# Kernel tuning notes

Measured on AMD Instinct MI355X. Metric: run time of the kernel, lower is better.

The kernel has to match this reference:

```python
import jax, jax.numpy as jnp
import numpy as np

GRID_SIZE = 5
SPLINE_ORDER = 3
NUM_COEFF = GRID_SIZE + SPLINE_ORDER  # 8
L = 3
B, I, H = 4096, 256, 512
EPS = 1e-5


def make_grid(in_features):
    # efficient-kan default grid over [-1, 1] extended by spline_order knots each side
    h = 2.0 / GRID_SIZE
    g = jnp.arange(-SPLINE_ORDER, GRID_SIZE + SPLINE_ORDER + 1, dtype=jnp.float32) * h - 1.0
    return jnp.broadcast_to(g, (in_features, g.shape[0]))  # (in, G+2k+1)


def b_splines(x, grid):
    # x: (B, in), grid: (in, G+2k+1) -> (B, in, G+k) via Cox-de-Boor recursion
    xg = x[..., None]
    bases = ((xg >= grid[:, :-1]) & (xg < grid[:, 1:])).astype(x.dtype)
    for j in range(1, SPLINE_ORDER + 1):
        left = (xg - grid[:, :-(j + 1)]) / (grid[:, j:-1] - grid[:, :-(j + 1)])
        right = (grid[:, j + 1:] - xg) / (grid[:, j + 1:] - grid[:, 1:-j])
        bases = left * bases[..., :-1] + right * bases[..., 1:]
    return bases


def kan_linear(x, base_w, spline_w, grid):
    # base path: SiLU(x) @ W_base^T ; spline path: sum over (in, coeff)
    base = jax.nn.silu(x) @ base_w.T
    spl = jnp.einsum('bik,oik->bo', b_splines(x, grid), spline_w)
    return base + spl


def layer_norm(x, g, b):
    mu = jnp.mean(x, axis=-1, keepdims=True)
    var = jnp.var(x, axis=-1, keepdims=True)
    return (x - mu) / jnp.sqrt(var + EPS) * g + b


def _sublayer(z_prev, wx_b, wx_s, wh_b, wh_s, hz_b, hz_s, phi_b, phi_s,
              hh_w, hh_b, ln_g, ln_b, x_t, grid_in, grid_h):
    s_t = kan_linear(x_t, wx_b, wx_s, grid_in) + kan_linear(z_prev, wh_b, wh_s, grid_h)
    o_t = kan_linear(s_t, phi_b, phi_s, grid_h)
    z_t = layer_norm(z_prev @ hh_w.T + hh_b + kan_linear(o_t, hz_b, hz_s, grid_h), ln_g, ln_b)
    return o_t, z_t


def setup_inputs() -> dict:
    key = jax.random.key(0)
    ks = jax.random.split(key, 24)
    s = 0.05  # small init to keep gates/splines in sane range
    inp = {
        'x_t': jax.random.normal(ks[0], (B, I), jnp.float32),
        'h_prev': jax.random.normal(ks[1], (B, H), jnp.float32),
        'c_prev': jax.random.normal(ks[2], (B, H), jnp.float32),
        'z_prev': jax.random.normal(ks[3], (L, B, H), jnp.float32),
        'wx_base': jax.random.normal(ks[4], (L, H, I), jnp.float32) * s,
        'wx_spline': jax.random.normal(ks[5], (L, H, I, NUM_COEFF), jnp.float32) * s,
        'wh_base': jax.random.normal(ks[6], (L, H, H), jnp.float32) * s,
        'wh_spline': jax.random.normal(ks[7], (L, H, H, NUM_COEFF), jnp.float32) * s,
        'hz_base': jax.random.normal(ks[8], (L, H, H), jnp.float32) * s,
        'hz_spline': jax.random.normal(ks[9], (L, H, H, NUM_COEFF), jnp.float32) * s,
        'phi_base': jax.random.normal(ks[10], (L, H, H), jnp.float32) * s,
        'phi_spline': jax.random.normal(ks[11], (L, H, H, NUM_COEFF), jnp.float32) * s,
        'hh_w': jax.random.normal(ks[12], (L, H, H), jnp.float32) * s,
        'hh_b': jax.random.normal(ks[13], (L, H), jnp.float32) * s,
        'ln_g': jnp.ones((L, H), jnp.float32),
        'ln_b': jnp.zeros((L, H), jnp.float32),
        'f_w': jax.random.normal(ks[14], (H, I + H), jnp.float32) * s,
        'f_b': jax.random.normal(ks[15], (H,), jnp.float32) * s,
        'i_w': jax.random.normal(ks[16], (H, I + H), jnp.float32) * s,
        'i_b': jax.random.normal(ks[17], (H,), jnp.float32) * s,
        'g_w': jax.random.normal(ks[18], (H, I + H), jnp.float32) * s,
        'g_b': jax.random.normal(ks[19], (H,), jnp.float32) * s,
        'o_w': jax.random.normal(ks[20], (H, L * H), jnp.float32) * s,
        'o_b': jax.random.normal(ks[21], (H,), jnp.float32) * s,
    }
    return inp


def reference(x_t, h_prev, c_prev, z_prev, wx_base, wx_spline, wh_base, wh_spline,
              hz_base, hz_spline, phi_base, phi_spline, hh_w, hh_b, ln_g, ln_b,
              f_w, f_b, i_w, i_b, g_w, g_b, o_w, o_b):
    grid_in = make_grid(I)
    grid_h = make_grid(H)
    cat = jnp.concatenate([x_t, h_prev], axis=-1)  # (B, I+H)
    f_t = jax.nn.sigmoid(cat @ f_w.T + f_b)
    i_t = jax.nn.sigmoid(cat @ i_w.T + i_b)
    g_t = jnp.tanh(cat @ g_w.T + g_b)
    # vmap the RKAN sublayer over the L stacked sublayers
    sub = jax.vmap(_sublayer, in_axes=(0,) * 13 + (None, None, None))
    o_all, z_all = sub(z_prev, wx_base, wx_spline, wh_base, wh_spline,
                       hz_base, hz_spline, phi_base, phi_spline,
                       hh_w, hh_b, ln_g, ln_b, x_t, grid_in, grid_h)
    # concat sublayer phi outputs: (L,B,H) -> (B, L*H)
    r_t = jnp.transpose(o_all, (1, 0, 2)).reshape(B, L * H)
    o_t = jax.nn.sigmoid(r_t @ o_w.T + o_b)
    c_t = f_t * c_prev + i_t * g_t
    h_t = o_t * jnp.tanh(c_t)
    return h_t, c_t, z_all
```

## Files before the change

kernel.cpp:

```cpp
#include <hip/hip_runtime.h>

typedef __attribute__((ext_vector_type(8))) short short8;
typedef __attribute__((ext_vector_type(4))) float floatx4;

__device__ inline short f2bf(float v) {
    unsigned u = __builtin_bit_cast(unsigned, v);
    unsigned r = (u + 0x7fffu + ((u >> 16) & 1u)) >> 16;
    return (short)r;
}
__device__ inline float bf2f(short s) {
    unsigned u = ((unsigned)(unsigned short)s) << 16;
    return __builtin_bit_cast(float, u);
}

__device__ inline void spline8(float v, short* arr) {
    float u = (v + 2.2f) * 2.5f;
    float fj = floorf(u);
    int jj = (int)fj;
    float t1 = u - fj;
    float ok = (jj >= 0 && jj <= 10) ? (1.f / 6.f) : 0.f;
    float t2 = t1 * t1, t3 = t2 * t1;
    float omt = 1.f - t1;
    short sw0 = f2bf(omt * omt * omt * ok);
    short sw1 = f2bf((3.f * t3 - 6.f * t2 + 4.f) * ok);
    short sw2 = f2bf((-3.f * t3 + 3.f * t2 + 3.f * t1 + 1.f) * ok);
    short sw3 = f2bf(t3 * ok);
#pragma unroll
    for (int s = 0; s < 8; ++s) {
        int rr = s - jj + 3;
        arr[s] = (rr == 0) ? sw0 : (rr == 1) ? sw1 : (rr == 2) ? sw2
                 : (rr == 3) ? sw3 : (short)0;
    }
}

__global__ __launch_bounds__(256, 3) void gemm128(
    int S, int Kh,
    const short* __restrict__ A0, int lda0, long sA0, int K0,
    const short* __restrict__ W0, int ldw0, long sW0,
    const short* __restrict__ A1, int lda1, long sA1, int K1,
    const short* __restrict__ W1, int ldw1, long sW1,
    float* __restrict__ C, int ldc, long sC, long sSplit)
{
    __shared__ short As[128 * 64];
    __shared__ short Ws[128 * 64];
    const int t = threadIdx.x;
    int n = blockIdx.x + (blockIdx.y << 5) + (blockIdx.z << 7);
    int k8 = n & 7, j = n >> 3;
    int byi = j & 3;
    int t2 = j >> 2;
    int bxi = k8 * 4 + (t2 & 3);
    int bzi = t2 >> 2;
    const int z = bzi / S, s = bzi % S;
    const int bm = bxi * 128, bn = byi * 128;
    const int lane = t & 63, w = t >> 6;
    const int wm = (w >> 1) * 64, wn = (w & 1) * 64;
    const int lrow = lane & 15, quad = lane >> 4;

    floatx4 acc[4][4] = {};

    const int kbeg = s * Kh, kend = kbeg + Kh;

    const short* A = A0 + (long)z * sA0;
    const short* W = W0 + (long)z * sW0;
    int lda = lda0, ldw = ldw0;
    int kb = kbeg, ke = (kend < K0) ? kend : K0;

    for (int seg = 0; seg < 2; ++seg) {
        for (int kv = kb; kv < ke; kv += 64) {
#pragma unroll
            for (int i = 0; i < 4; ++i) {
                int c = i * 256 + t;
                int row = c >> 3;
                int cg = ((c ^ row) & 7) * 8;
                const short* gp = A + (long)(bm + row) * lda + kv + cg;
                __builtin_amdgcn_global_load_lds(
                    (const __attribute__((address_space(1))) void*)gp,
                    (__attribute__((address_space(3))) void*)(As + c * 8), 16, 0, 0);
                const short* gq = W + (long)(bn + row) * ldw + kv + cg;
                __builtin_amdgcn_global_load_lds(
                    (const __attribute__((address_space(1))) void*)gq,
                    (__attribute__((address_space(3))) void*)(Ws + c * 8), 16, 0, 0);
            }
            __syncthreads();
#pragma unroll
            for (int kk = 0; kk < 2; ++kk) {
                short8 af[4], bfr[4];
#pragma unroll
                for (int mi = 0; mi < 4; ++mi) {
                    int r = wm + mi * 16 + lrow;
                    af[mi] = *(const short8*)(As + r * 64 +
                                              (((kk * 4 + quad) ^ (r & 7)) * 8));
                }
#pragma unroll
                for (int ni = 0; ni < 4; ++ni) {
                    int r = wn + ni * 16 + lrow;
                    bfr[ni] = *(const short8*)(Ws + r * 64 +
                                               (((kk * 4 + quad) ^ (r & 7)) * 8));
                }
#pragma unroll
                for (int mi = 0; mi < 4; ++mi)
#pragma unroll
                    for (int ni = 0; ni < 4; ++ni)
                        acc[mi][ni] = __builtin_amdgcn_mfma_f32_16x16x32_bf16(
                            af[mi], bfr[ni], acc[mi][ni], 0, 0, 0);
            }
            __syncthreads();
        }
        A = A1 + (long)z * sA1;
        W = W1 + (long)z * sW1;
        lda = lda1; ldw = ldw1;
        kb = ((kbeg > K0) ? kbeg : K0) - K0;
        ke = kend - K0;
    }

    float* Cz = C + (long)z * sC + (long)s * sSplit;
#pragma unroll
    for (int mi = 0; mi < 4; ++mi)
#pragma unroll
        for (int ni = 0; ni < 4; ++ni)
#pragma unroll
            for (int r = 0; r < 4; ++r) {
                int row = bm + wm + mi * 16 + quad * 4 + r;
                int col = bn + wn + ni * 16 + lrow;
                Cz[(long)row * ldc + col] = acc[mi][ni][r];
            }
}

__global__ __launch_bounds__(256) void gemm64(
    int swz,
    const short* __restrict__ A0, int lda0, long sA0, int K0,
    const short* __restrict__ W0, int ldw0, long sW0,
    const short* __restrict__ A1, int lda1, long sA1, int K1,
    const short* __restrict__ W1, int ldw1, long sW1,
    short* __restrict__ C, int ldc, long sC)
{
    __shared__ short As[64 * 32];
    __shared__ short Ws[128 * 32];
    const int t = threadIdx.x;
    int bxi = blockIdx.x, byi = blockIdx.y, bzi = blockIdx.z;
    if (swz) {
        int n = bxi + (byi << 6) + (bzi << 8);
        int k = n & 7, j = n >> 3;
        byi = j & 3;
        bxi = k * 8 + ((j >> 2) & 7);
        bzi = j >> 5;
    }
    const int z = bzi;
    const int bm = bxi * 64;
    const int bn = byi * 128;
    const int lane = t & 63, w = t >> 6;
    const int wm = (w >> 1) * 32, wn = (w & 1) * 64;
    const int lrow = lane & 15, quad = lane >> 4;

    floatx4 acc[2][4] = {};

    const short* A = A0 + (long)z * sA0;
    const short* W = W0 + (long)z * sW0;
    int K = K0, lda = lda0, ldw = ldw0;

    for (int seg = 0; seg < 2; ++seg) {
        for (int k0 = 0; k0 < K; k0 += 32) {
            {
                int row = t >> 2, cg = (t & 3) * 8;
                const short* gp = A + (long)(bm + row) * lda + k0 + cg;
                __builtin_amdgcn_global_load_lds(
                    (const __attribute__((address_space(1))) void*)gp,
                    (__attribute__((address_space(3))) void*)(As + t * 8), 16, 0, 0);
            }
#pragma unroll
            for (int j = 0; j < 2; ++j) {
                int cj = j * 256 + t;
                int row = cj >> 2, cg = (cj & 3) * 8;
                const short* gq = W + (long)(bn + row) * ldw + k0 + cg;
                __builtin_amdgcn_global_load_lds(
                    (const __attribute__((address_space(1))) void*)gq,
                    (__attribute__((address_space(3))) void*)(Ws + cj * 8), 16, 0, 0);
            }
            __syncthreads();
            short8 af[2], bfr[4];
#pragma unroll
            for (int mi = 0; mi < 2; ++mi)
                af[mi] = *(const short8*)(As + (wm + mi * 16 + lrow) * 32 + quad * 8);
#pragma unroll
            for (int ni = 0; ni < 4; ++ni)
                bfr[ni] = *(const short8*)(Ws + (wn + ni * 16 + lrow) * 32 + quad * 8);
#pragma unroll
            for (int mi = 0; mi < 2; ++mi)
#pragma unroll
                for (int ni = 0; ni < 4; ++ni)
                    acc[mi][ni] = __builtin_amdgcn_mfma_f32_16x16x32_bf16(
                        af[mi], bfr[ni], acc[mi][ni], 0, 0, 0);
            __syncthreads();
        }
        A = A1 + (long)z * sA1; W = W1 + (long)z * sW1;
        K = K1; lda = lda1; ldw = ldw1;
    }

    short* Cz = C + (long)z * sC;
#pragma unroll
    for (int mi = 0; mi < 2; ++mi)
#pragma unroll
        for (int ni = 0; ni < 4; ++ni)
#pragma unroll
            for (int r = 0; r < 4; ++r) {
                int row = bm + wm + mi * 16 + quad * 4 + r;
                int col = bn + wn + ni * 16 + lrow;
                Cz[(long)row * ldc + col] = f2bf(acc[mi][ni][r]);
            }
}

__global__ __launch_bounds__(256) void megapack4(
    const float* __restrict__ wx_b, const float* __restrict__ wx_s,
    const float* __restrict__ wh_b, const float* __restrict__ wh_s,
    const float* __restrict__ hz_b, const float* __restrict__ hz_s,
    const float* __restrict__ phi_b, const float* __restrict__ phi_s,
    const float* __restrict__ hh_w, const float* __restrict__ o_w,
    const float* __restrict__ f_w, const float* __restrict__ i_w,
    const float* __restrict__ g_w,
    short* __restrict__ Wx, short* __restrict__ Wh, short* __restrict__ Whz,
    short* __restrict__ Wphi, short* __restrict__ HHb, short* __restrict__ OWb,
    short* __restrict__ Wg)
{
    int bid = blockIdx.x, tid = threadIdx.x;
    float4 v;
    short* dst;
    long e;
    if (bid < 3456) {
        e = ((long)bid * 256 + tid) * 4;
        int r = (int)(e / 2304), c = (int)(e % 2304);
        v = (c < 256) ? *(const float4*)(wx_b + (long)r * 256 + c)
                      : *(const float4*)(wx_s + (long)r * 2048 + (c - 256));
        dst = Wx + e;
    } else if (bid < 24192) {
        int jb = bid - 3456;
        int job = jb / 6912, lb = jb % 6912;
        const float* bp = (job == 0) ? wh_b : (job == 1) ? hz_b : phi_b;
        const float* sp = (job == 0) ? wh_s : (job == 1) ? hz_s : phi_s;
        short* dp = (job == 0) ? Wh : (job == 1) ? Whz : Wphi;
        e = ((long)lb * 256 + tid) * 4;
        int r = (int)(e / 4608), c = (int)(e % 4608);
        v = (c < 512) ? *(const float4*)(bp + (long)r * 512 + c)
                      : *(const float4*)(sp + (long)r * 4096 + (c - 512));
        dst = dp + e;
    } else if (bid < 24960) {
        e = ((long)(bid - 24192) * 256 + tid) * 4;
        v = *(const float4*)(hh_w + e);
        dst = HHb + e;
    } else if (bid < 25728) {
        e = ((long)(bid - 24960) * 256 + tid) * 4;
        v = *(const float4*)(o_w + e);
        dst = OWb + e;
    } else if (bid < 26112) {
        e = ((long)(bid - 25728) * 256 + tid) * 4;
        v = *(const float4*)(f_w + e);
        dst = Wg + e;
    } else if (bid < 26496) {
        e = ((long)(bid - 26112) * 256 + tid) * 4;
        v = *(const float4*)(i_w + e);
        dst = Wg + 393216 + e;
    } else {
        e = ((long)(bid - 26496) * 256 + tid) * 4;
        v = *(const float4*)(g_w + e);
        dst = Wg + 786432 + e;
    }
    dst[0] = f2bf(v.x); dst[1] = f2bf(v.y);
    dst[2] = f2bf(v.z); dst[3] = f2bf(v.w);
}

__global__ __launch_bounds__(256) void prep_acts(
    const float* __restrict__ x_t, const float* __restrict__ h_prev,
    const float* __restrict__ z_prev,
    short* __restrict__ Xe, short* __restrict__ Agate,
    short* __restrict__ Ze, short* __restrict__ zraw)
{
    int bid = blockIdx.x, tid = threadIdx.x;
    if (bid < 4096) {
        int r = bid, i = tid;
        float v = x_t[(long)r * 256 + i];
        Agate[(long)r * 768 + i] = f2bf(v);
        long ob = (long)r * 2304;
        Xe[ob + i] = f2bf(v / (1.f + __expf(-v)));
        short arr[8];
        spline8(v, arr);
        *(short8*)(Xe + ob + 256 + (long)i * 8) = *(const short8*)arr;
    } else if (bid < 12288) {
        long idx = (long)(bid - 4096) * 256 + tid;
        long b = idx >> 9; int hh = (int)(idx & 511);
        Agate[b * 768 + 256 + hh] = f2bf(h_prev[idx]);
    } else {
        int j = bid - 12288;
        int r = j >> 1, i = (j & 1) * 256 + tid;
        float v = z_prev[(long)r * 512 + i];
        zraw[(long)r * 512 + i] = f2bf(v);
        long ob = (long)r * 4608;
        Ze[ob + i] = f2bf(v / (1.f + __expf(-v)));
        short arr[8];
        spline8(v, arr);
        *(short8*)(Ze + ob + 512 + (long)i * 8) = *(const short8*)arr;
    }
}

__global__ __launch_bounds__(256) void expand_pair(
    const float* __restrict__ P, long sSplit, int S, int inF,
    short* __restrict__ out, short* __restrict__ compact)
{
    int i = (blockIdx.x * 256 + threadIdx.x) * 2;
    int r = blockIdx.y;
    long idx = (long)r * inF + i;
    float2 v = *(const float2*)(P + idx);
    for (int s = 1; s < S; ++s) {
        float2 a = *(const float2*)(P + idx + (long)s * sSplit);
        v.x += a.x; v.y += a.y;
    }
    if (compact) { compact[idx] = f2bf(v.x); compact[idx + 1] = f2bf(v.y); }

    long ob = (long)r * inF * 9;
    out[ob + i]     = f2bf(v.x / (1.f + __expf(-v.x)));
    out[ob + i + 1] = f2bf(v.y / (1.f + __expf(-v.y)));

    short arr[8];
    spline8(v.x, arr);
    *(short8*)(out + ob + inF + (long)i * 8) = *(const short8*)arr;
    spline8(v.y, arr);
    *(short8*)(out + ob + inF + (long)(i + 1) * 8) = *(const short8*)arr;
}

__global__ __launch_bounds__(256) void ln_wave(const float* __restrict__ P,
                                               long sSplit, int S,
                                               const float* __restrict__ hh_b,
                                               const float* __restrict__ ln_g,
                                               const float* __restrict__ ln_b,
                                               float* __restrict__ out)
{
    int wv = threadIdx.x >> 6, lane = threadIdx.x & 63;
    int row = blockIdx.x * 4 + wv;
    int l = row >> 12;
    int col = lane * 8;
    long base = (long)row * 512 + col;
    float v[8];
#pragma unroll
    for (int e = 0; e < 8; ++e) v[e] = hh_b[l * 512 + col + e];
    for (int s = 0; s < S; ++s) {
        float4 a = *(const float4*)(P + base + (long)s * sSplit);
        float4 b = *(const float4*)(P + base + 4 + (long)s * sSplit);
        v[0] += a.x; v[1] += a.y; v[2] += a.z; v[3] += a.w;
        v[4] += b.x; v[5] += b.y; v[6] += b.z; v[7] += b.w;
    }
    float sm = 0.f, sq = 0.f;
#pragma unroll
    for (int e = 0; e < 8; ++e) { sm += v[e]; sq += v[e] * v[e]; }
#pragma unroll
    for (int off = 32; off; off >>= 1) {
        sm += __shfl_down(sm, off);
        sq += __shfl_down(sq, off);
    }
    sm = __shfl(sm, 0);
    sq = __shfl(sq, 0);
    float mu = sm * (1.f / 512.f);
    float var = sq * (1.f / 512.f) - mu * mu;
    float rstd = rsqrtf(var + 1e-5f);
    float o[8];
#pragma unroll
    for (int e = 0; e < 8; ++e)
        o[e] = (v[e] - mu) * rstd * ln_g[l * 512 + col + e] + ln_b[l * 512 + col + e];
    float* op = out + base;
    *(float4*)op = make_float4(o[0], o[1], o[2], o[3]);
    *(float4*)(op + 4) = make_float4(o[4], o[5], o[6], o[7]);
}

__global__ __launch_bounds__(256) void cell_epilogue(const short* __restrict__ gates,
                                                     const short* __restrict__ opre,
                                                     const float* __restrict__ c_prev,
                                                     const float* __restrict__ f_b,
                                                     const float* __restrict__ i_b,
                                                     const float* __restrict__ g_b,
                                                     const float* __restrict__ o_b,
                                                     float* __restrict__ out)
{
    long idx = blockIdx.x * 256L + threadIdx.x;
    long b = idx >> 9; int h = (int)(idx & 511);
    const short* g = gates + b * 1536;
    float fp = bf2f(g[h]) + f_b[h];
    float ip = bf2f(g[512 + h]) + i_b[h];
    float gp = bf2f(g[1024 + h]) + g_b[h];
    float op = bf2f(opre[idx]) + o_b[h];
    float ft = 1.f / (1.f + __expf(-fp));
    float it = 1.f / (1.f + __expf(-ip));
    float gt = tanhf(gp);
    float ot = 1.f / (1.f + __expf(-op));
    float c = ft * c_prev[idx] + it * gt;
    out[idx] = ot * tanhf(c);
    out[idx + 2097152] = c;
}

extern "C" void kernel_launch(void* const* d_in, const int* in_sizes, int n_in,
                              void* d_out, int out_size, void* d_ws, size_t ws_size,
                              hipStream_t stream)
{
    const float* x_t       = (const float*)d_in[0];
    const float* h_prev    = (const float*)d_in[1];
    const float* c_prev    = (const float*)d_in[2];
    const float* z_prev    = (const float*)d_in[3];
    const float* wx_base   = (const float*)d_in[4];
    const float* wx_spline = (const float*)d_in[5];
    const float* wh_base   = (const float*)d_in[6];
    const float* wh_spline = (const float*)d_in[7];
    const float* hz_base   = (const float*)d_in[8];
    const float* hz_spline = (const float*)d_in[9];
    const float* phi_base  = (const float*)d_in[10];
    const float* phi_spline= (const float*)d_in[11];
    const float* hh_w      = (const float*)d_in[12];
    const float* hh_b      = (const float*)d_in[13];
    const float* ln_g      = (const float*)d_in[14];
    const float* ln_b      = (const float*)d_in[15];
    const float* f_w       = (const float*)d_in[16];
    const float* f_b       = (const float*)d_in[17];
    const float* i_w       = (const float*)d_in[18];
    const float* i_b       = (const float*)d_in[19];
    const float* g_w       = (const float*)d_in[20];
    const float* g_b       = (const float*)d_in[21];
    const float* o_w       = (const float*)d_in[22];
    const float* o_b       = (const float*)d_in[23];
    float* out = (float*)d_out;
    const long BH = 4096L * 512;

    char* p = (char*)d_ws;
    auto alloc = [&](size_t bytes) {
        char* q = p;
        p += (bytes + 255) & ~(size_t)255;
        return q;
    };

    short* Wx   = (short*)alloc(3L * 512 * 2304 * 2);
    short* Wh   = (short*)alloc(3L * 512 * 4608 * 2);
    short* Whz  = (short*)alloc(3L * 512 * 4608 * 2);
    short* Wphi = (short*)alloc(3L * 512 * 4608 * 2);
    short* HHb  = (short*)alloc(3L * 512 * 512 * 2);
    short* OWb  = (short*)alloc(512L * 1536 * 2);
    short* Wg   = (short*)alloc(1536L * 768 * 2);
    short* Agate= (short*)alloc(4096L * 768 * 2);
    short* zraw = (short*)alloc(3L * 4096 * 512 * 2);
    short* XR   = (short*)alloc(4096L * 2304 * 2);
    short* Ebuf = (short*)alloc(3L * 4096 * 4608 * 2);

    const int S = 2;
    const long PS = 3L * 4096 * 512;
    float* Pbuf = (float*)alloc((size_t)S * PS * 4);

    short* Xe = XR;
    short* Rbuf = XR;
    short* gbuf = Ebuf;
    short* opre = Ebuf + 4096L * 1536;

    megapack4<<<26880, 256, 0, stream>>>(
        wx_base, wx_spline, wh_base, wh_spline, hz_base, hz_spline,
        phi_base, phi_spline, hh_w, o_w, f_w, i_w, g_w,
        Wx, Wh, Whz, Wphi, HHb, OWb, Wg);

    prep_acts<<<36864, 256, 0, stream>>>(x_t, h_prev, z_prev, Xe, Agate, Ebuf, zraw);

    gemm128<<<dim3(32, 4, 3 * S), 256, 0, stream>>>(S, 3456,
        Xe, 2304, 0, 2304,                 Wx, 2304, 512L * 2304,
        Ebuf, 4608, 4096L * 4608, 4608,    Wh, 4608, 512L * 4608,
        Pbuf, 512, 4096L * 512, PS);

    expand_pair<<<dim3(1, 12288), 256, 0, stream>>>(Pbuf, PS, S, 512, Ebuf, (short*)0);

    gemm128<<<dim3(32, 4, 3 * S), 256, 0, stream>>>(S, 2304,
        Ebuf, 4608, 4096L * 4608, 4608,    Wphi, 4608, 512L * 4608,
        zraw, 0, 0, 0,                     Wphi, 0, 0,
        Pbuf, 1536, 512, PS);

    expand_pair<<<dim3(1, 12288), 256, 0, stream>>>(Pbuf, PS, S, 512, Ebuf, Rbuf);

    gemm128<<<dim3(32, 4, 3 * S), 256, 0, stream>>>(S, 2560,
        Ebuf, 13824, 4608, 4608,           Whz, 4608, 512L * 4608,
        zraw, 512, 4096L * 512, 512,       HHb, 512, 512L * 512,
        Pbuf, 512, 4096L * 512, PS);

    ln_wave<<<3072, 256, 0, stream>>>(Pbuf, PS, S, hh_b, ln_g, ln_b, out + 2 * BH);

    gemm64<<<dim3(64, 12, 1), 256, 0, stream>>>(0,
        Agate, 768, 0, 768,  Wg, 768, 0,
        Agate, 768, 0, 0,    Wg, 768, 0,
        gbuf, 1536, 0);

    gemm64<<<dim3(64, 4, 1), 256, 0, stream>>>(0,
        Rbuf, 1536, 0, 1536, OWb, 1536, 0,
        Rbuf, 1536, 0, 0,    OWb, 1536, 0,
        opre, 512, 0);

    cell_epilogue<<<8192, 256, 0, stream>>>(gbuf, opre, c_prev, f_b, i_b, g_b, o_b, out);
}
```

Before: 695.5 us.

## Vectorize pack/prep/expand kernels and widen gemm64 K-tile with swizzled LDS

The weight pack kernel now converts 8 floats per thread. The activation prep and expand kernels now process 4 elements per thread, using float4 loads and short4/short8 stores. This cuts block count and improves memory transaction width for these bandwidth-bound elementwise stages. gemm64 drops its unused second segment, doubles the K tile to 64 and XOR-swizzles its LDS layout to reduce bank conflicts, which halves the number of barriers per K. In exchange it uses more shared memory per block.

```diff
diff --git a/kernel.cpp b/kernel.cpp
--- a/kernel.cpp
+++ b/kernel.cpp
@@ -1,6 +1,7 @@
 #include <hip/hip_runtime.h>
 
 typedef __attribute__((ext_vector_type(8))) short short8;
+typedef __attribute__((ext_vector_type(4))) short short4v;
 typedef __attribute__((ext_vector_type(4))) float floatx4;
 
 __device__ inline short f2bf(float v) {
@@ -11,6 +12,19 @@
 __device__ inline float bf2f(short s) {
     unsigned u = ((unsigned)(unsigned short)s) << 16;
     return __builtin_bit_cast(float, u);
+}
+__device__ inline short4v pack4(float4 v) {
+    short4v o;
+    o[0] = f2bf(v.x); o[1] = f2bf(v.y); o[2] = f2bf(v.z); o[3] = f2bf(v.w);
+    return o;
+}
+__device__ inline short4v silu4(float4 v) {
+    float4 s;
+    s.x = v.x / (1.f + __expf(-v.x));
+    s.y = v.y / (1.f + __expf(-v.y));
+    s.z = v.z / (1.f + __expf(-v.z));
+    s.w = v.w / (1.f + __expf(-v.w));
+    return pack4(s);
 }
 
 __device__ inline void spline8(float v, short* arr) {
@@ -31,6 +45,14 @@
         arr[s] = (rr == 0) ? sw0 : (rr == 1) ? sw1 : (rr == 2) ? sw2
                  : (rr == 3) ? sw3 : (short)0;
     }
+}
+__device__ inline void expand4(float4 v, short* silu_dst, short* spl_dst) {
+    *(short4v*)silu_dst = silu4(v);
+    short arr[8];
+    spline8(v.x, arr); *(short8*)(spl_dst)      = *(const short8*)arr;
+    spline8(v.y, arr); *(short8*)(spl_dst + 8)  = *(const short8*)arr;
+    spline8(v.z, arr); *(short8*)(spl_dst + 16) = *(const short8*)arr;
+    spline8(v.w, arr); *(short8*)(spl_dst + 24) = *(const short8*)arr;
 }
 
 __global__ __launch_bounds__(256, 3) void gemm128(
@@ -127,27 +149,16 @@
 }
 
 __global__ __launch_bounds__(256) void gemm64(
-    int swz,
     const short* __restrict__ A0, int lda0, long sA0, int K0,
     const short* __restrict__ W0, int ldw0, long sW0,
-    const short* __restrict__ A1, int lda1, long sA1, int K1,
-    const short* __restrict__ W1, int ldw1, long sW1,
     short* __restrict__ C, int ldc, long sC)
 {
-    __shared__ short As[64 * 32];
-    __shared__ short Ws[128 * 32];
+    __shared__ short As[64 * 64];
+    __shared__ short Ws[128 * 64];
     const int t = threadIdx.x;
-    int bxi = blockIdx.x, byi = blockIdx.y, bzi = blockIdx.z;
-    if (swz) {
-        int n = bxi + (byi << 6) + (bzi << 8);
-        int k = n & 7, j = n >> 3;
-        byi = j & 3;
-        bxi = k * 8 + ((j >> 2) & 7);
-        bzi = j >> 5;
-    }
-    const int z = bzi;
-    const int bm = bxi * 64;
-    const int bn = byi * 128;
+    const int z = blockIdx.z;
+    const int bm = blockIdx.x * 64;
+    const int bn = blockIdx.y * 128;
     const int lane = t & 63, w = t >> 6;
     const int wm = (w >> 1) * 32, wn = (w & 1) * 64;
     const int lrow = lane & 15, quad = lane >> 4;
@@ -156,44 +167,52 @@
 
     const short* A = A0 + (long)z * sA0;
     const short* W = W0 + (long)z * sW0;
-    int K = K0, lda = lda0, ldw = ldw0;
-
-    for (int seg = 0; seg < 2; ++seg) {
-        for (int k0 = 0; k0 < K; k0 += 32) {
-            {
-                int row = t >> 2, cg = (t & 3) * 8;
-                const short* gp = A + (long)(bm + row) * lda + k0 + cg;
-                __builtin_amdgcn_global_load_lds(
-                    (const __attribute__((address_space(1))) void*)gp,
-                    (__attribute__((address_space(3))) void*)(As + t * 8), 16, 0, 0);
+
+    for (int k0 = 0; k0 < K0; k0 += 64) {
+#pragma unroll
+        for (int i = 0; i < 2; ++i) {
+            int c = i * 256 + t;
+            int row = c >> 3;
+            int cg = ((c ^ row) & 7) * 8;
+            const short* gp = A + (long)(bm + row) * lda0 + k0 + cg;
+            __builtin_amdgcn_global_load_lds(
+                (const __attribute__((address_space(1))) void*)gp,
+                (__attribute__((address_space(3))) void*)(As + c * 8), 16, 0, 0);
+        }
+#pragma unroll
+        for (int i = 0; i < 4; ++i) {
+            int c = i * 256 + t;
+            int row = c >> 3;
+            int cg = ((c ^ row) & 7) * 8;
+            const short* gq = W + (long)(bn + row) * ldw0 + k0 + cg;
+            __builtin_amdgcn_global_load_lds(
+                (const __attribute__((address_space(1))) void*)gq,
+                (__attribute__((address_space(3))) void*)(Ws + c * 8), 16, 0, 0);
+        }
+        __syncthreads();
+#pragma unroll
+        for (int kk = 0; kk < 2; ++kk) {
+            short8 af[2], bfr[4];
+#pragma unroll
+            for (int mi = 0; mi < 2; ++mi) {
+                int r = wm + mi * 16 + lrow;
+                af[mi] = *(const short8*)(As + r * 64 +
+                                          (((kk * 4 + quad) ^ (r & 7)) * 8));
             }
 #pragma unroll
-            for (int j = 0; j < 2; ++j) {
-                int cj = j * 256 + t;
-                int row = cj >> 2, cg = (cj & 3) * 8;
-                const short* gq = W + (long)(bn + row) * ldw + k0 + cg;
-                __builtin_amdgcn_global_load_lds(
-                    (const __attribute__((address_space(1))) void*)gq,
-                    (__attribute__((address_space(3))) void*)(Ws + cj * 8), 16, 0, 0);
+            for (int ni = 0; ni < 4; ++ni) {
+                int r = wn + ni * 16 + lrow;
+                bfr[ni] = *(const short8*)(Ws + r * 64 +
+                                           (((kk * 4 + quad) ^ (r & 7)) * 8));
             }
-            __syncthreads();
-            short8 af[2], bfr[4];
-#pragma unroll
-            for (int mi = 0; mi < 2; ++mi)
-                af[mi] = *(const short8*)(As + (wm + mi * 16 + lrow) * 32 + quad * 8);
-#pragma unroll
-            for (int ni = 0; ni < 4; ++ni)
-                bfr[ni] = *(const short8*)(Ws + (wn + ni * 16 + lrow) * 32 + quad * 8);
 #pragma unroll
             for (int mi = 0; mi < 2; ++mi)
 #pragma unroll
                 for (int ni = 0; ni < 4; ++ni)
                     acc[mi][ni] = __builtin_amdgcn_mfma_f32_16x16x32_bf16(
                         af[mi], bfr[ni], acc[mi][ni], 0, 0, 0);
-            __syncthreads();
         }
-        A = A1 + (long)z * sA1; W = W1 + (long)z * sW1;
-        K = K1; lda = lda1; ldw = ldw1;
+        __syncthreads();
     }
 
     short* Cz = C + (long)z * sC;
@@ -209,7 +228,7 @@
             }
 }
 
-__global__ __launch_bounds__(256) void megapack4(
+__global__ __launch_bounds__(256) void megapack8(
     const float* __restrict__ wx_b, const float* __restrict__ wx_s,
     const float* __restrict__ wh_b, const float* __restrict__ wh_s,
     const float* __restrict__ hz_b, const float* __restrict__ hz_s,
@@ -222,107 +241,96 @@
     short* __restrict__ Wg)
 {
     int bid = blockIdx.x, tid = threadIdx.x;
-    float4 v;
+    const float* sp;
     short* dst;
     long e;
-    if (bid < 3456) {
-        e = ((long)bid * 256 + tid) * 4;
+    if (bid < 1728) {
+        e = ((long)bid * 256 + tid) * 8;
         int r = (int)(e / 2304), c = (int)(e % 2304);
-        v = (c < 256) ? *(const float4*)(wx_b + (long)r * 256 + c)
-                      : *(const float4*)(wx_s + (long)r * 2048 + (c - 256));
+        sp = (c < 256) ? wx_b + (long)r * 256 + c
+                       : wx_s + (long)r * 2048 + (c - 256);
         dst = Wx + e;
-    } else if (bid < 24192) {
-        int jb = bid - 3456;
-        int job = jb / 6912, lb = jb % 6912;
+    } else if (bid < 12096) {
+        int jb = bid - 1728;
+        int job = jb / 3456, lb = jb % 3456;
         const float* bp = (job == 0) ? wh_b : (job == 1) ? hz_b : phi_b;
-        const float* sp = (job == 0) ? wh_s : (job == 1) ? hz_s : phi_s;
+        const float* spw = (job == 0) ? wh_s : (job == 1) ? hz_s : phi_s;
         short* dp = (job == 0) ? Wh : (job == 1) ? Whz : Wphi;
-        e = ((long)lb * 256 + tid) * 4;
+        e = ((long)lb * 256 + tid) * 8;
         int r = (int)(e / 4608), c = (int)(e % 4608);
-        v = (c < 512) ? *(const float4*)(bp + (long)r * 512 + c)
-                      : *(const float4*)(sp + (long)r * 4096 + (c - 512));
+        sp = (c < 512) ? bp + (long)r * 512 + c
+                       : spw + (long)r * 4096 + (c - 512);
         dst = dp + e;
-    } else if (bid < 24960) {
-        e = ((long)(bid - 24192) * 256 + tid) * 4;
-        v = *(const float4*)(hh_w + e);
-        dst = HHb + e;
-    } else if (bid < 25728) {
-        e = ((long)(bid - 24960) * 256 + tid) * 4;
-        v = *(const float4*)(o_w + e);
-        dst = OWb + e;
-    } else if (bid < 26112) {
-        e = ((long)(bid - 25728) * 256 + tid) * 4;
-        v = *(const float4*)(f_w + e);
-        dst = Wg + e;
-    } else if (bid < 26496) {
-        e = ((long)(bid - 26112) * 256 + tid) * 4;
-        v = *(const float4*)(i_w + e);
-        dst = Wg + 393216 + e;
+    } else if (bid < 12480) {
+        e = ((long)(bid - 12096) * 256 + tid) * 8;
+        sp = hh_w + e; dst = HHb + e;
+    } else if (bid < 12864) {
+        e = ((long)(bid - 12480) * 256 + tid) * 8;
+        sp = o_w + e; dst = OWb + e;
+    } else if (bid < 13056) {
+        e = ((long)(bid - 12864) * 256 + tid) * 8;
+        sp = f_w + e; dst = Wg + e;
+    } else if (bid < 13248) {
+        e = ((long)(bid - 13056) * 256 + tid) * 8;
+        sp = i_w + e; dst = Wg + 393216 + e;
     } else {
-        e = ((long)(bid - 26496) * 256 + tid) * 4;
-        v = *(const float4*)(g_w + e);
-        dst = Wg + 786432 + e;
-    }
-    dst[0] = f2bf(v.x); dst[1] = f2bf(v.y);
-    dst[2] = f2bf(v.z); dst[3] = f2bf(v.w);
-}
-
-__global__ __launch_bounds__(256) void prep_acts(
+        e = ((long)(bid - 13248) * 256 + tid) * 8;
+        sp = g_w + e; dst = Wg + 786432 + e;
+    }
+    float4 a = *(const float4*)sp;
+    float4 b = *(const float4*)(sp + 4);
+    short8 o;
+    o[0] = f2bf(a.x); o[1] = f2bf(a.y); o[2] = f2bf(a.z); o[3] = f2bf(a.w);
+    o[4] = f2bf(b.x); o[5] = f2bf(b.y); o[6] = f2bf(b.z); o[7] = f2bf(b.w);
+    *(short8*)dst = o;
+}
+
+__global__ __launch_bounds__(256) void prep_acts4(
     const float* __restrict__ x_t, const float* __restrict__ h_prev,
     const float* __restrict__ z_prev,
     short* __restrict__ Xe, short* __restrict__ Agate,
     short* __restrict__ Ze, short* __restrict__ zraw)
 {
     int bid = blockIdx.x, tid = threadIdx.x;
-    if (bid < 4096) {
-        int r = bid, i = tid;
-        float v = x_t[(long)r * 256 + i];
-        Agate[(long)r * 768 + i] = f2bf(v);
+    if (bid < 1024) {
+        int r = (bid << 2) + (tid >> 6);
+        int i = (tid & 63) << 2;
+        float4 v = *(const float4*)(x_t + (long)r * 256 + i);
+        *(short4v*)(Agate + (long)r * 768 + i) = pack4(v);
         long ob = (long)r * 2304;
-        Xe[ob + i] = f2bf(v / (1.f + __expf(-v)));
-        short arr[8];
-        spline8(v, arr);
-        *(short8*)(Xe + ob + 256 + (long)i * 8) = *(const short8*)arr;
-    } else if (bid < 12288) {
-        long idx = (long)(bid - 4096) * 256 + tid;
+        expand4(v, Xe + ob + i, Xe + ob + 256 + (long)i * 8);
+    } else if (bid < 3072) {
+        long idx = ((long)(bid - 1024) * 256 + tid) * 4;
+        float4 v = *(const float4*)(h_prev + idx);
         long b = idx >> 9; int hh = (int)(idx & 511);
-        Agate[b * 768 + 256 + hh] = f2bf(h_prev[idx]);
+        *(short4v*)(Agate + b * 768 + 256 + hh) = pack4(v);
     } else {
-        int j = bid - 12288;
-        int r = j >> 1, i = (j & 1) * 256 + tid;
-        float v = z_prev[(long)r * 512 + i];
-        zraw[(long)r * 512 + i] = f2bf(v);
+        int j = bid - 3072;
+        int r = (j << 1) + (tid >> 7);
+        int i = (tid & 127) << 2;
+        float4 v = *(const float4*)(z_prev + (long)r * 512 + i);
+        *(short4v*)(zraw + (long)r * 512 + i) = pack4(v);
         long ob = (long)r * 4608;
-        Ze[ob + i] = f2bf(v / (1.f + __expf(-v)));
-        short arr[8];
-        spline8(v, arr);
-        *(short8*)(Ze + ob + 512 + (long)i * 8) = *(const short8*)arr;
-    }
-}
-
-__global__ __launch_bounds__(256) void expand_pair(
-    const float* __restrict__ P, long sSplit, int S, int inF,
+        expand4(v, Ze + ob + i, Ze + ob + 512 + (long)i * 8);
+    }
+}
+
+__global__ __launch_bounds__(256) void expand_pair4(
+    const float* __restrict__ P, long sSplit, int S,
     short* __restrict__ out, short* __restrict__ compact)
 {
-    int i = (blockIdx.x * 256 + threadIdx.x) * 2;
-    int r = blockIdx.y;
-    long idx = (long)r * inF + i;
-    float2 v = *(const float2*)(P + idx);
+    int tid = threadIdx.x;
+    int r = (blockIdx.x << 1) + (tid >> 7);
+    int i = (tid & 127) << 2;
+    long idx = (long)r * 512 + i;
+    float4 v = *(const float4*)(P + idx);
     for (int s = 1; s < S; ++s) {
-        float2 a = *(const float2*)(P + idx + (long)s * sSplit);
-        v.x += a.x; v.y += a.y;
-    }
-    if (compact) { compact[idx] = f2bf(v.x); compact[idx + 1] = f2bf(v.y); }
-
-    long ob = (long)r * inF * 9;
-    out[ob + i]     = f2bf(v.x / (1.f + __expf(-v.x)));
-    out[ob + i + 1] = f2bf(v.y / (1.f + __expf(-v.y)));
-
-    short arr[8];
-    spline8(v.x, arr);
-    *(short8*)(out + ob + inF + (long)i * 8) = *(const short8*)arr;
-    spline8(v.y, arr);
-    *(short8*)(out + ob + inF + (long)(i + 1) * 8) = *(const short8*)arr;
+        float4 a = *(const float4*)(P + idx + (long)s * sSplit);
+        v.x += a.x; v.y += a.y; v.z += a.z; v.w += a.w;
+    }
+    if (compact) *(short4v*)(compact + idx) = pack4(v);
+    long ob = (long)r * 4608;
+    expand4(v, out + ob + i, out + ob + 512 + (long)i * 8);
 }
 
 __global__ __launch_bounds__(256) void ln_wave(const float* __restrict__ P,
@@ -452,26 +460,26 @@
     short* gbuf = Ebuf;
     short* opre = Ebuf + 4096L * 1536;
 
-    megapack4<<<26880, 256, 0, stream>>>(
+    megapack8<<<13440, 256, 0, stream>>>(
         wx_base, wx_spline, wh_base, wh_spline, hz_base, hz_spline,
         phi_base, phi_spline, hh_w, o_w, f_w, i_w, g_w,
         Wx, Wh, Whz, Wphi, HHb, OWb, Wg);
 
-    prep_acts<<<36864, 256, 0, stream>>>(x_t, h_prev, z_prev, Xe, Agate, Ebuf, zraw);
+    prep_acts4<<<9216, 256, 0, stream>>>(x_t, h_prev, z_prev, Xe, Agate, Ebuf, zraw);
 
     gemm128<<<dim3(32, 4, 3 * S), 256, 0, stream>>>(S, 3456,
         Xe, 2304, 0, 2304,                 Wx, 2304, 512L * 2304,
         Ebuf, 4608, 4096L * 4608, 4608,    Wh, 4608, 512L * 4608,
         Pbuf, 512, 4096L * 512, PS);
 
-    expand_pair<<<dim3(1, 12288), 256, 0, stream>>>(Pbuf, PS, S, 512, Ebuf, (short*)0);
+    expand_pair4<<<6144, 256, 0, stream>>>(Pbuf, PS, S, Ebuf, (short*)0);
 
     gemm128<<<dim3(32, 4, 3 * S), 256, 0, stream>>>(S, 2304,
         Ebuf, 4608, 4096L * 4608, 4608,    Wphi, 4608, 512L * 4608,
         zraw, 0, 0, 0,                     Wphi, 0, 0,
         Pbuf, 1536, 512, PS);
 
-    expand_pair<<<dim3(1, 12288), 256, 0, stream>>>(Pbuf, PS, S, 512, Ebuf, Rbuf);
+    expand_pair4<<<6144, 256, 0, stream>>>(Pbuf, PS, S, Ebuf, Rbuf);
 
     gemm128<<<dim3(32, 4, 3 * S), 256, 0, stream>>>(S, 2560,
         Ebuf, 13824, 4608, 4608,           Whz, 4608, 512L * 4608,
@@ -480,14 +488,12 @@
 
     ln_wave<<<3072, 256, 0, stream>>>(Pbuf, PS, S, hh_b, ln_g, ln_b, out + 2 * BH);
 
-    gemm64<<<dim3(64, 12, 1), 256, 0, stream>>>(0,
+    gemm64<<<dim3(64, 12, 1), 256, 0, stream>>>(
         Agate, 768, 0, 768,  Wg, 768, 0,
-        Agate, 768, 0, 0,    Wg, 768, 0,
         gbuf, 1536, 0);
 
-    gemm64<<<dim3(64, 4, 1), 256, 0, stream>>>(0,
+    gemm64<<<dim3(64, 4, 1), 256, 0, stream>>>(
         Rbuf, 1536, 0, 1536, OWb, 1536, 0,
-        Rbuf, 1536, 0, 0,    OWb, 1536, 0,
         opre, 512, 0);
 
     cell_epilogue<<<8192, 256, 0, stream>>>(gbuf, opre, c_prev, f_b, i_b, g_b, o_b, out);
```

New measurement: 705.3 us. No clear change (+1.4%).
